# Kernel optimization log

Hardware: AMD Instinct MI355X
Metric: run time of the kernel (lower is better)

The kernel has to match this reference:

```python
import jax, jax.numpy as jnp
import numpy as np

B, H, W, C = 64, 512, 512, 3


def _warp_one(img, Minv):
    # img: (H, W, C). cv2.warpPerspective: dst(x,y) = src(Minv @ [x, y, 1])
    Hh, Ww = img.shape[0], img.shape[1]
    ys, xs = jnp.meshgrid(jnp.arange(Hh, dtype=jnp.float32),
                          jnp.arange(Ww, dtype=jnp.float32), indexing='ij')
    pts = jnp.stack([xs, ys, jnp.ones_like(xs)], 0)          # (3, H, W)
    src = jnp.einsum('ij,jhw->ihw', Minv, pts)               # (3, H, W)
    u = src[0] / src[2]                                      # source x coord
    v = src[1] / src[2]                                      # source y coord
    x0 = jnp.floor(u)
    y0 = jnp.floor(v)
    wx = u - x0
    wy = v - y0
    x0i = x0.astype(jnp.int32)
    y0i = y0.astype(jnp.int32)

    def tap(yi, xi):
        # BORDER_CONSTANT = 0: out-of-range taps contribute zero
        valid = (xi >= 0) & (xi < Ww) & (yi >= 0) & (yi < Hh)
        val = img[jnp.clip(yi, 0, Hh - 1), jnp.clip(xi, 0, Ww - 1)]
        return jnp.where(valid[..., None], val, jnp.zeros((), img.dtype))

    out = (tap(y0i,     x0i    ) * ((1.0 - wy) * (1.0 - wx))[..., None]
         + tap(y0i,     x0i + 1) * ((1.0 - wy) * wx)[..., None]
         + tap(y0i + 1, x0i    ) * (wy * (1.0 - wx))[..., None]
         + tap(y0i + 1, x0i + 1) * (wy * wx)[..., None])
    return out


def setup_inputs() -> dict:
    key = jax.random.key(0)
    imgs = jax.random.normal(key, (B, H, W, C), dtype=jnp.float32)
    M = jnp.array([[1.05, 0.12, 8.0],
                   [0.08, 0.98, -5.0],
                   [2e-4, 1e-4, 1.0]], dtype=jnp.float32)
    return {"imgs": imgs, "M": M}


def reference(imgs, M):
    Minv = jnp.linalg.inv(M)
    return jax.vmap(lambda im: _warp_one(im, Minv))(imgs)
```

## Files before the change

### kernel.cpp

```cpp
#include <hip/hip_runtime.h>

#define BATCH 64
#define IMH 512
#define IMW 512
#define NCH 3

__global__ void invert_m_kernel(const float* __restrict__ M, float* __restrict__ Minv) {
    if (threadIdx.x != 0 || blockIdx.x != 0) return;
    double a = M[0], b = M[1], c = M[2];
    double d = M[3], e = M[4], f = M[5];
    double g = M[6], h = M[7], i = M[8];
    double A =  (e * i - f * h);
    double Bq = -(d * i - f * g);
    double Cq =  (d * h - e * g);
    double det = a * A + b * Bq + c * Cq;
    double inv_det = 1.0 / det;
    Minv[0] = (float)(A * inv_det);
    Minv[1] = (float)(-(b * i - c * h) * inv_det);
    Minv[2] = (float)((b * f - c * e) * inv_det);
    Minv[3] = (float)(Bq * inv_det);
    Minv[4] = (float)((a * i - c * g) * inv_det);
    Minv[5] = (float)(-(a * f - c * d) * inv_det);
    Minv[6] = (float)(Cq * inv_det);
    Minv[7] = (float)(-(a * h - b * g) * inv_det);
    Minv[8] = (float)((a * e - b * d) * inv_det);
}

__global__ __launch_bounds__(256) void warp_kernel(const float* __restrict__ img,
                                                   const float* __restrict__ Minv,
                                                   float* __restrict__ out) {
    const int idx = blockIdx.x * blockDim.x + threadIdx.x;
    const int x = idx & (IMW - 1);
    const int y = (idx >> 9) & (IMH - 1);
    const int b = idx >> 18;

    const float m0 = Minv[0], m1 = Minv[1], m2 = Minv[2];
    const float m3 = Minv[3], m4 = Minv[4], m5 = Minv[5];
    const float m6 = Minv[6], m7 = Minv[7], m8 = Minv[8];

    const float fx = (float)x, fy = (float)y;
    const float s0 = m0 * fx + m1 * fy + m2;
    const float s1 = m3 * fx + m4 * fy + m5;
    const float s2 = m6 * fx + m7 * fy + m8;
    const float u = s0 / s2;
    const float v = s1 / s2;

    const float x0f = floorf(u);
    const float y0f = floorf(v);
    const float wx = u - x0f;
    const float wy = v - y0f;
    const int x0 = (int)x0f;
    const int y0 = (int)y0f;
    const int x1 = x0 + 1;
    const int y1 = y0 + 1;

    float w00 = (1.0f - wy) * (1.0f - wx);
    float w01 = (1.0f - wy) * wx;
    float w10 = wy * (1.0f - wx);
    float w11 = wy * wx;

    const bool vx0 = (x0 >= 0) & (x0 < IMW);
    const bool vx1 = (x1 >= 0) & (x1 < IMW);
    const bool vy0 = (y0 >= 0) & (y0 < IMH);
    const bool vy1 = (y1 >= 0) & (y1 < IMH);
    w00 = (vy0 & vx0) ? w00 : 0.0f;
    w01 = (vy0 & vx1) ? w01 : 0.0f;
    w10 = (vy1 & vx0) ? w10 : 0.0f;
    w11 = (vy1 & vx1) ? w11 : 0.0f;

    const int x0c = min(max(x0, 0), IMW - 1);
    const int x1c = min(max(x1, 0), IMW - 1);
    const int y0c = min(max(y0, 0), IMH - 1);
    const int y1c = min(max(y1, 0), IMH - 1);

    const float* base = img + (size_t)b * (IMH * IMW * NCH);
    const float* p00 = base + ((size_t)y0c * IMW + x0c) * NCH;
    const float* p01 = base + ((size_t)y0c * IMW + x1c) * NCH;
    const float* p10 = base + ((size_t)y1c * IMW + x0c) * NCH;
    const float* p11 = base + ((size_t)y1c * IMW + x1c) * NCH;

    float acc0 = w00 * p00[0] + w01 * p01[0] + w10 * p10[0] + w11 * p11[0];
    float acc1 = w00 * p00[1] + w01 * p01[1] + w10 * p10[1] + w11 * p11[1];
    float acc2 = w00 * p00[2] + w01 * p01[2] + w10 * p10[2] + w11 * p11[2];

    float* o = out + (size_t)idx * NCH;
    o[0] = acc0;
    o[1] = acc1;
    o[2] = acc2;
}

extern "C" void kernel_launch(void* const* d_in, const int* in_sizes, int n_in,
                              void* d_out, int out_size, void* d_ws, size_t ws_size,
                              hipStream_t stream) {
    const float* imgs = (const float*)d_in[0];
    const float* M = (const float*)d_in[1];
    float* out = (float*)d_out;
    float* minv = (float*)d_ws;

    invert_m_kernel<<<1, 64, 0, stream>>>(M, minv);

    const int total = BATCH * IMH * IMW;
    warp_kernel<<<total / 256, 256, 0, stream>>>(imgs, minv, out);
}
```

Measured before the change: 332.0 us.

## Fuse matrix inversion into warp kernel and reuse coordinates across batch images

Drops the separate inversion launch; each thread now inverts M itself in double precision. Each thread computes sampling coordinates and weights once and loops over 16 images in its group, so per-pixel math is amortised across the batch. Neighbouring taps are loaded as contiguous 24-byte rows using a clamped base x with remapped weights, outputs go through nontemporal stores, and the divide is replaced by a hardware reciprocal. The trade-offs are fewer blocks (4096) with a serial per-thread loop, redundant per-thread double-precision inversion, and slight precision loss from the approximate reciprocal.

```diff
diff --git a/kernel.cpp b/kernel.cpp
--- a/kernel.cpp
+++ b/kernel.cpp
@@ -4,89 +4,88 @@
 #define IMH 512
 #define IMW 512
 #define NCH 3
-
-__global__ void invert_m_kernel(const float* __restrict__ M, float* __restrict__ Minv) {
-    if (threadIdx.x != 0 || blockIdx.x != 0) return;
-    double a = M[0], b = M[1], c = M[2];
-    double d = M[3], e = M[4], f = M[5];
-    double g = M[6], h = M[7], i = M[8];
-    double A =  (e * i - f * h);
-    double Bq = -(d * i - f * g);
-    double Cq =  (d * h - e * g);
-    double det = a * A + b * Bq + c * Cq;
-    double inv_det = 1.0 / det;
-    Minv[0] = (float)(A * inv_det);
-    Minv[1] = (float)(-(b * i - c * h) * inv_det);
-    Minv[2] = (float)((b * f - c * e) * inv_det);
-    Minv[3] = (float)(Bq * inv_det);
-    Minv[4] = (float)((a * i - c * g) * inv_det);
-    Minv[5] = (float)(-(a * f - c * d) * inv_det);
-    Minv[6] = (float)(Cq * inv_det);
-    Minv[7] = (float)(-(a * h - b * g) * inv_det);
-    Minv[8] = (float)((a * e - b * d) * inv_det);
-}
+#define IMSZ (IMH * IMW * NCH)
+#define NPIX (IMH * IMW)
+#define GROUPS 4
+#define BPG (BATCH / GROUPS)
 
 __global__ __launch_bounds__(256) void warp_kernel(const float* __restrict__ img,
-                                                   const float* __restrict__ Minv,
+                                                   const float* __restrict__ Mp,
                                                    float* __restrict__ out) {
-    const int idx = blockIdx.x * blockDim.x + threadIdx.x;
-    const int x = idx & (IMW - 1);
-    const int y = (idx >> 9) & (IMH - 1);
-    const int b = idx >> 18;
+    const int bid = blockIdx.x;
+    const int g = bid & (GROUPS - 1);
+    const int pix = ((bid >> 2) << 8) | threadIdx.x;
+    const int x = pix & (IMW - 1);
+    const int y = pix >> 9;
 
-    const float m0 = Minv[0], m1 = Minv[1], m2 = Minv[2];
-    const float m3 = Minv[3], m4 = Minv[4], m5 = Minv[5];
-    const float m6 = Minv[6], m7 = Minv[7], m8 = Minv[8];
+    double a = Mp[0], b = Mp[1], c = Mp[2];
+    double d = Mp[3], e = Mp[4], f = Mp[5];
+    double gg = Mp[6], h = Mp[7], i = Mp[8];
+    double A  =  (e * i - f * h);
+    double Bq = -(d * i - f * gg);
+    double Cq =  (d * h - e * gg);
+    double invdet = 1.0 / (a * A + b * Bq + c * Cq);
+    const float m0 = (float)(A * invdet);
+    const float m1 = (float)(-(b * i - c * h) * invdet);
+    const float m2 = (float)((b * f - c * e) * invdet);
+    const float m3 = (float)(Bq * invdet);
+    const float m4 = (float)((a * i - c * gg) * invdet);
+    const float m5 = (float)(-(a * f - c * d) * invdet);
+    const float m6 = (float)(Cq * invdet);
+    const float m7 = (float)(-(a * h - b * gg) * invdet);
+    const float m8 = (float)((a * e - b * d) * invdet);
 
     const float fx = (float)x, fy = (float)y;
-    const float s0 = m0 * fx + m1 * fy + m2;
-    const float s1 = m3 * fx + m4 * fy + m5;
-    const float s2 = m6 * fx + m7 * fy + m8;
-    const float u = s0 / s2;
-    const float v = s1 / s2;
+    const float s0 = fmaf(m0, fx, fmaf(m1, fy, m2));
+    const float s1 = fmaf(m3, fx, fmaf(m4, fy, m5));
+    const float s2 = fmaf(m6, fx, fmaf(m7, fy, m8));
+    const float r2 = __builtin_amdgcn_rcpf(s2);
+    const float u = s0 * r2;
+    const float v = s1 * r2;
 
-    const float x0f = floorf(u);
-    const float y0f = floorf(v);
-    const float wx = u - x0f;
-    const float wy = v - y0f;
-    const int x0 = (int)x0f;
-    const int y0 = (int)y0f;
-    const int x1 = x0 + 1;
-    const int y1 = y0 + 1;
+    const float x0f = floorf(u), y0f = floorf(v);
+    const float wx = u - x0f,   wy = v - y0f;
+    const int x0 = (int)x0f, y0 = (int)y0f;
+    const int x1 = x0 + 1,   y1 = y0 + 1;
 
-    float w00 = (1.0f - wy) * (1.0f - wx);
-    float w01 = (1.0f - wy) * wx;
-    float w10 = wy * (1.0f - wx);
-    float w11 = wy * wx;
-
-    const bool vx0 = (x0 >= 0) & (x0 < IMW);
-    const bool vx1 = (x1 >= 0) & (x1 < IMW);
-    const bool vy0 = (y0 >= 0) & (y0 < IMH);
-    const bool vy1 = (y1 >= 0) & (y1 < IMH);
-    w00 = (vy0 & vx0) ? w00 : 0.0f;
-    w01 = (vy0 & vx1) ? w01 : 0.0f;
-    w10 = (vy1 & vx0) ? w10 : 0.0f;
-    w11 = (vy1 & vx1) ? w11 : 0.0f;
-
-    const int x0c = min(max(x0, 0), IMW - 1);
-    const int x1c = min(max(x1, 0), IMW - 1);
+    const int xb  = min(max(x0, 0), IMW - 2);
     const int y0c = min(max(y0, 0), IMH - 1);
     const int y1c = min(max(y1, 0), IMH - 1);
 
-    const float* base = img + (size_t)b * (IMH * IMW * NCH);
-    const float* p00 = base + ((size_t)y0c * IMW + x0c) * NCH;
-    const float* p01 = base + ((size_t)y0c * IMW + x1c) * NCH;
-    const float* p10 = base + ((size_t)y1c * IMW + x0c) * NCH;
-    const float* p11 = base + ((size_t)y1c * IMW + x1c) * NCH;
+    const float w0x = (x0 >= 0 && x0 < IMW) ? (1.0f - wx) : 0.0f;
+    const float w1x = (x1 >= 0 && x1 < IMW) ? wx : 0.0f;
+    const float b0 = (x0 == xb     ? w0x : 0.0f) + (x1 == xb     ? w1x : 0.0f);
+    const float b1 = (x0 == xb + 1 ? w0x : 0.0f) + (x1 == xb + 1 ? w1x : 0.0f);
+    const float wy0 = (y0 >= 0 && y0 < IMH) ? (1.0f - wy) : 0.0f;
+    const float wy1 = (y1 >= 0 && y1 < IMH) ? wy : 0.0f;
 
-    float acc0 = w00 * p00[0] + w01 * p01[0] + w10 * p10[0] + w11 * p11[0];
-    float acc1 = w00 * p00[1] + w01 * p01[1] + w10 * p10[1] + w11 * p11[1];
-    float acc2 = w00 * p00[2] + w01 * p01[2] + w10 * p10[2] + w11 * p11[2];
+    const float c00 = wy0 * b0, c01 = wy0 * b1;
+    const float c10 = wy1 * b0, c11 = wy1 * b1;
 
-    float* o = out + (size_t)idx * NCH;
-    o[0] = acc0;
-    o[1] = acc1;
-    o[2] = acc2;
+    const size_t off0 = ((size_t)y0c * IMW + xb) * NCH;
+    const size_t off1 = ((size_t)y1c * IMW + xb) * NCH;
+    const float* p0 = img + (size_t)g * BPG * IMSZ + off0;
+    const float* p1 = img + (size_t)g * BPG * IMSZ + off1;
+    float* o = out + ((size_t)g * BPG * NPIX + pix) * NCH;
+
+    #pragma unroll 4
+    for (int t = 0; t < BPG; ++t) {
+        float r0[6], r1[6];
+        __builtin_memcpy(r0, p0, 24);
+        __builtin_memcpy(r1, p1, 24);
+
+        const float o0 = c00 * r0[0] + c01 * r0[3] + c10 * r1[0] + c11 * r1[3];
+        const float o1 = c00 * r0[1] + c01 * r0[4] + c10 * r1[1] + c11 * r1[4];
+        const float o2 = c00 * r0[2] + c01 * r0[5] + c10 * r1[2] + c11 * r1[5];
+
+        __builtin_nontemporal_store(o0, o + 0);
+        __builtin_nontemporal_store(o1, o + 1);
+        __builtin_nontemporal_store(o2, o + 2);
+
+        p0 += IMSZ;
+        p1 += IMSZ;
+        o  += (size_t)NPIX * NCH;
+    }
 }
 
 extern "C" void kernel_launch(void* const* d_in, const int* in_sizes, int n_in,
@@ -95,10 +94,7 @@
     const float* imgs = (const float*)d_in[0];
     const float* M = (const float*)d_in[1];
     float* out = (float*)d_out;
-    float* minv = (float*)d_ws;
 
-    invert_m_kernel<<<1, 64, 0, stream>>>(M, minv);
-
-    const int total = BATCH * IMH * IMW;
-    warp_kernel<<<total / 256, 256, 0, stream>>>(imgs, minv, out);
+    const int blocks = (NPIX / 256) * GROUPS;
+    warp_kernel<<<blocks, 256, 0, stream>>>(imgs, M, out);
 }
```

New measurement: 353.2 us. +6.4%, slower.
